# Kernel tuning notes

Measured on AMD Instinct MI355X. Metric: run time of the kernel, lower is better.

The kernel has to match this reference:

```python
import math
import jax, jax.numpy as jnp
import numpy as np

N, D, E, H = 4096, 512, 64, 8
LN_EPS = 1e-5


def setup_inputs() -> dict:
    key = jax.random.key(0)
    ks = jax.random.split(key, 6)
    return {
        "x": jax.random.normal(ks[0], (N, D), jnp.float32),
        "wq": jax.random.normal(ks[1], (H, D, E), jnp.float32) * 0.05,
        "wk": jax.random.normal(ks[2], (H, D, E), jnp.float32) * 0.05,
        "wv": jax.random.normal(ks[3], (H, D, E), jnp.float32) * 0.05,
        "w_mh": jax.random.normal(ks[4], (H * E, D), jnp.float32) * 0.05,
        "ln1_g": jnp.ones((D,), jnp.float32),
        "ln1_b": jnp.zeros((D,), jnp.float32),
        "ffn_w": jax.random.normal(ks[5], (D, D), jnp.float32) * 0.05,  # torch Linear weight [out,in]
        "ffn_b": jnp.zeros((D,), jnp.float32),
        "ln2_g": jnp.ones((D,), jnp.float32),
        "ln2_b": jnp.zeros((D,), jnp.float32),
    }


def _layernorm(y, g, b):
    m = y.mean(-1, keepdims=True)
    v = ((y - m) ** 2).mean(-1, keepdims=True)
    return (y - m) * jax.lax.rsqrt(v + LN_EPS) * g + b


def reference(x, wq, wk, wv, w_mh, ln1_g, ln1_b, ffn_w, ffn_b, ln2_g, ln2_b):
    dk = math.sqrt(wk.shape[-1])  # sqrt(embedding_size), as in the torch code
    q = jnp.einsum('nd,hde->hne', x, wq)  # [H,N,E]
    k = jnp.einsum('nd,hde->hne', x, wk)
    v = jnp.einsum('nd,hde->hne', x, wv)
    scores = jax.nn.softmax(jnp.einsum('hne,hme->hnm', q, k) / dk, axis=-1)  # [H,N,N]
    z = jnp.einsum('hnm,hme->hne', scores, v)  # [H,N,E]
    concat_z = jnp.transpose(z, (1, 0, 2)).reshape(x.shape[0], -1)  # [N, H*E]
    transformed_z = concat_z @ w_mh  # [N, D]
    normed_z = _layernorm(transformed_z + x, ln1_g, ln1_b)
    out = normed_z @ ffn_w.T + ffn_b  # nn.Linear
    return _layernorm(out + normed_z, ln2_g, ln2_b)
```

## Files before the change

### kernel.cpp

```cpp
#include <hip/hip_runtime.h>

#define NN 4096
#define DD 512
#define EE 64
#define HH 8

typedef _Float16 f16;
typedef f16 f16x4 __attribute__((ext_vector_type(4)));
typedef f16 f16x8 __attribute__((ext_vector_type(8)));
typedef float f32x4 __attribute__((ext_vector_type(4)));

__device__ __forceinline__ float hexp2(float x) { return __builtin_amdgcn_exp2f(x); }

__device__ void tile_transpose_cvt(const float* __restrict__ src, f16* __restrict__ dst,
                                   int R, int C, int bx, int by, int tid)
{
    __shared__ float t[32][33];
    const int tx = tid & 31, ty = tid >> 5;
    #pragma unroll
    for (int i = 0; i < 4; ++i) {
        int r = ty + i * 8;
        t[r][tx] = src[(size_t)(by + r) * C + bx + tx];
    }
    __syncthreads();
    #pragma unroll
    for (int i = 0; i < 4; ++i) {
        int c = ty + i * 8;
        dst[(size_t)(bx + c) * R + by + tx] = (f16)t[tx][c];
    }
}

__global__ __launch_bounds__(256) void prep_kernel(
    const float* __restrict__ x, const float* __restrict__ ffn_w,
    const float* __restrict__ wq, const float* __restrict__ wk, const float* __restrict__ wv,
    const float* __restrict__ w_mh,
    f16* __restrict__ xh, f16* __restrict__ ffnT, f16* __restrict__ wqkvT, f16* __restrict__ wmhT)
{
    const int job = blockIdx.y;
    const int tid = threadIdx.x;
    if (job == 0) {
        size_t i = ((size_t)blockIdx.x * 256 + tid) * 4;
        const size_t step = (size_t)256 * 256 * 4;
        for (; i < (size_t)NN * DD; i += step) {
            float4 t = *(const float4*)(x + i);
            f16x4 h = { (f16)t.x, (f16)t.y, (f16)t.z, (f16)t.w };
            *(f16x4*)(xh + i) = h;
        }
    } else if (job == 1) {
        size_t i = ((size_t)blockIdx.x * 256 + tid) * 4;
        float4 t = *(const float4*)(ffn_w + i);
        f16x4 h = { (f16)t.x, (f16)t.y, (f16)t.z, (f16)t.w };
        *(f16x4*)(ffnT + i) = h;
    } else if (job <= 4) {
        const float* src = (job == 2) ? wq : (job == 3) ? wk : wv;
        f16* dst = wqkvT + (size_t)(job - 2) * HH * EE * DD;
        const int z = blockIdx.x >> 5;
        const int tile = blockIdx.x & 31;
        tile_transpose_cvt(src + (size_t)z * DD * EE, dst + (size_t)z * DD * EE,
                           DD, EE, (tile & 1) * 32, (tile >> 1) * 32, tid);
    } else {
        const int tile = blockIdx.x;
        tile_transpose_cvt(w_mh, wmhT, DD, DD, (tile & 15) * 32, (tile >> 4) * 32, tid);
    }
}

__global__ __launch_bounds__(256) void qkv_mfma_kernel(
    const f16* __restrict__ A, const f16* __restrict__ BT,
    f16* __restrict__ qh, f16* __restrict__ kh, f16* __restrict__ vTh)
{
    __shared__ f16 As[64][72];
    __shared__ f16 Bs[64][72];
    const int tid = threadIdx.x;
    const int n0 = blockIdx.x * 64;
    const int cb = blockIdx.y;
    const int sel = cb >> 3, h = cb & 7;
    const f16* Arow = A + (size_t)n0 * DD;
    const f16* Brow = BT + (size_t)cb * 64 * DD;

    const int lane = tid & 63, wave = tid >> 6;
    const int l16 = lane & 15, quad = lane >> 4;
    const int m0 = wave * 16;

    f32x4 acc[4];
    #pragma unroll
    for (int t = 0; t < 4; ++t) acc[t] = (f32x4){0.f, 0.f, 0.f, 0.f};

    for (int kt = 0; kt < DD; kt += 64) {
        __syncthreads();
        #pragma unroll
        for (int i = 0; i < 2; ++i) {
            int idx = tid + i * 256;
            int r = idx >> 3, c8 = (idx & 7) * 8;
            *(f16x8*)(&As[r][c8]) = *(const f16x8*)(Arow + (size_t)r * DD + kt + c8);
            *(f16x8*)(&Bs[r][c8]) = *(const f16x8*)(Brow + (size_t)r * DD + kt + c8);
        }
        __syncthreads();
        #pragma unroll
        for (int kk = 0; kk < 64; kk += 32) {
            f16x8 a = *(const f16x8*)(&As[m0 + l16][kk + quad * 8]);
            #pragma unroll
            for (int t = 0; t < 4; ++t) {
                f16x8 b = *(const f16x8*)(&Bs[t * 16 + l16][kk + quad * 8]);
                acc[t] = __builtin_amdgcn_mfma_f32_16x16x32_f16(a, b, acc[t], 0, 0, 0);
            }
        }
    }

    if (sel == 2) {
        #pragma unroll
        for (int t = 0; t < 4; ++t) {
            int e = t * 16 + l16;
            #pragma unroll
            for (int r = 0; r < 4; ++r)
                vTh[((size_t)h * EE + e) * NN + n0 + m0 + quad * 4 + r] = (f16)acc[t][r];
        }
    } else {
        f16* o = (sel == 0) ? qh : kh;
        const float s = (sel == 0) ? 0.125f * 1.44269504088896f : 1.0f;
        #pragma unroll
        for (int r = 0; r < 4; ++r) {
            int row = n0 + m0 + quad * 4 + r;
            #pragma unroll
            for (int t = 0; t < 4; ++t)
                o[(size_t)h * NN * EE + (size_t)row * EE + t * 16 + l16] = (f16)(acc[t][r] * s);
        }
    }
}

#define BQ 128
#define BK 64
#define LK (BK + 12)

__global__ __launch_bounds__(256) void attn_mfma_kernel(
    const f16* __restrict__ q, const f16* __restrict__ k,
    const f16* __restrict__ vT, float* __restrict__ Opart, float* __restrict__ lpart)
{
    __shared__ f16 Ks[BK][LK];
    __shared__ f16 VsT[EE][LK];

    const int tid = threadIdx.x;
    const int h = blockIdx.y;
    const int n0 = blockIdx.x * BQ;
    const int sp = blockIdx.z;
    const int nsp = gridDim.z;
    const int wave = tid >> 6;
    const int lane = tid & 63;
    const int l16 = lane & 15;
    const int quad = lane >> 4;
    const int m0 = wave * 16;

    const f16* qh = q + (size_t)h * NN * EE;
    const f16* kh = k + (size_t)h * NN * EE;
    const f16* vh = vT + (size_t)h * NN * EE;

    f16x8 qf[2][2];
    #pragma unroll
    for (int s = 0; s < 2; ++s) {
        const f16* qb = qh + (size_t)(n0 + s * 64 + m0 + l16) * EE;
        qf[s][0] = *(const f16x8*)(qb + quad * 8);
        qf[s][1] = *(const f16x8*)(qb + 32 + quad * 8);
    }

    float lp[2] = {0.f, 0.f};
    f32x4 O[2][4];
    #pragma unroll
    for (int s = 0; s < 2; ++s)
        #pragma unroll
        for (int t = 0; t < 4; ++t) O[s][t] = (f32x4){0.f, 0.f, 0.f, 0.f};

    const int span = NN / nsp;
    const int k_begin = sp * span;
    const int k_end = k_begin + span;

    const int srow = tid >> 3, sc8 = (tid & 7) * 8;
    const int srow2 = (tid + 256) >> 3, sc82 = ((tid + 256) & 7) * 8;
    #define KPERM(kk_) (((kk_) & 0x23) | (((kk_) & 0x04) << 2) | (((kk_) & 0x18) >> 1))
    const int prow1 = KPERM(srow), prow2 = KPERM(srow2);

    f16x8 kr0 = *(const f16x8*)(kh + (size_t)(k_begin + srow) * EE + sc8);
    f16x8 kr1 = *(const f16x8*)(kh + (size_t)(k_begin + srow2) * EE + sc82);
    f16x8 vr0 = *(const f16x8*)(vh + (size_t)srow * NN + k_begin + sc8);
    f16x8 vr1 = *(const f16x8*)(vh + (size_t)srow2 * NN + k_begin + sc82);

    for (int kt = k_begin; kt < k_end; kt += BK) {
        __syncthreads();
        *(f16x8*)(&Ks[prow1][sc8]) = kr0;
        *(f16x8*)(&Ks[prow2][sc82]) = kr1;
        *(f16x8*)(&VsT[srow][sc8]) = vr0;
        *(f16x8*)(&VsT[srow2][sc82]) = vr1;
        __syncthreads();

        if (kt + BK < k_end) {
            kr0 = *(const f16x8*)(kh + (size_t)(kt + BK + srow) * EE + sc8);
            kr1 = *(const f16x8*)(kh + (size_t)(kt + BK + srow2) * EE + sc82);
            vr0 = *(const f16x8*)(vh + (size_t)srow * NN + kt + BK + sc8);
            vr1 = *(const f16x8*)(vh + (size_t)srow2 * NN + kt + BK + sc82);
        }

        f16x8 bf[2][2];
        #pragma unroll
        for (int t = 0; t < 4; ++t) {
            f16x8 a0 = *(const f16x8*)(&Ks[t * 16 + l16][quad * 8]);
            f16x8 a1 = *(const f16x8*)(&Ks[t * 16 + l16][32 + quad * 8]);
            #pragma unroll
            for (int s = 0; s < 2; ++s) {
                f32x4 st = {0.f, 0.f, 0.f, 0.f};
                st = __builtin_amdgcn_mfma_f32_16x16x32_f16(a0, qf[s][0], st, 0, 0, 0);
                st = __builtin_amdgcn_mfma_f32_16x16x32_f16(a1, qf[s][1], st, 0, 0, 0);
                float p0 = hexp2(st[0]);
                float p1 = hexp2(st[1]);
                float p2 = hexp2(st[2]);
                float p3 = hexp2(st[3]);
                lp[s] += (p0 + p1) + (p2 + p3);
                f16x8& b = bf[s][t >> 1];
                const int o = (t & 1) * 4;
                b[o + 0] = (f16)p0; b[o + 1] = (f16)p1;
                b[o + 2] = (f16)p2; b[o + 3] = (f16)p3;
            }
        }

        #pragma unroll
        for (int te = 0; te < 4; ++te) {
            f16x8 v0 = *(const f16x8*)(&VsT[te * 16 + l16][quad * 8]);
            f16x8 v1 = *(const f16x8*)(&VsT[te * 16 + l16][32 + quad * 8]);
            #pragma unroll
            for (int s = 0; s < 2; ++s) {
                O[s][te] = __builtin_amdgcn_mfma_f32_16x16x32_f16(v0, bf[s][0], O[s][te], 0, 0, 0);
                O[s][te] = __builtin_amdgcn_mfma_f32_16x16x32_f16(v1, bf[s][1], O[s][te], 0, 0, 0);
            }
        }
    }

    #pragma unroll
    for (int s = 0; s < 2; ++s) {
        float l = lp[s];
        l += __shfl_xor(l, 16);
        l += __shfl_xor(l, 32);
        const int row = n0 + s * 64 + m0 + l16;
        if (quad == 0)
            lpart[(size_t)sp * HH * NN + (size_t)h * NN + row] = l;
        float* obase = Opart + ((size_t)sp * NN + row) * DD + h * EE;
        #pragma unroll
        for (int te = 0; te < 4; ++te)
            *(f32x4*)(obase + te * 16 + quad * 4) = O[s][te];
    }
}

__global__ __launch_bounds__(256) void attn_combine_kernel(
    const float* __restrict__ Opart, const float* __restrict__ lpart, f16* __restrict__ zh, int nsp)
{
    const size_t idx = ((size_t)blockIdx.x * 256 + threadIdx.x) * 8;
    const int n = (int)(idx >> 9);
    const int h = (int)((idx & 511) >> 6);
    float l = 0.f;
    for (int s = 0; s < nsp; ++s) l += lpart[(size_t)s * HH * NN + (size_t)h * NN + n];
    const float inv = 1.f / l;
    f32x4 a0 = {0.f,0.f,0.f,0.f}, a1 = {0.f,0.f,0.f,0.f};
    for (int s = 0; s < nsp; ++s) {
        a0 += *(const f32x4*)(Opart + (size_t)s * NN * DD + idx);
        a1 += *(const f32x4*)(Opart + (size_t)s * NN * DD + idx + 4);
    }
    f16x8 o;
    #pragma unroll
    for (int i = 0; i < 4; ++i) {
        o[i]     = (f16)(a0[i] * inv);
        o[i + 4] = (f16)(a1[i] * inv);
    }
    *(f16x8*)(zh + idx) = o;
}

__global__ __launch_bounds__(256) void gemm_mfma_kernel(
    const f16* __restrict__ A, const f16* __restrict__ BT,
    const float* __restrict__ bias, const float* __restrict__ resid32,
    const f16* __restrict__ resid16, float* __restrict__ out)
{
    __shared__ f16 As[64][72];
    __shared__ f16 Bs[64][72];
    const int tid = threadIdx.x;
    const int n0 = blockIdx.x * 64;
    const int j0 = blockIdx.y * 64;
    const f16* Arow = A + (size_t)n0 * DD;
    const f16* Brow = BT + (size_t)j0 * DD;

    const int lane = tid & 63, wave = tid >> 6;
    const int l16 = lane & 15, quad = lane >> 4;
    const int m0 = wave * 16;

    f32x4 acc[4];
    #pragma unroll
    for (int t = 0; t < 4; ++t) acc[t] = (f32x4){0.f, 0.f, 0.f, 0.f};

    for (int kt = 0; kt < DD; kt += 64) {
        __syncthreads();
        #pragma unroll
        for (int i = 0; i < 2; ++i) {
            int idx = tid + i * 256;
            int r = idx >> 3, c8 = (idx & 7) * 8;
            *(f16x8*)(&As[r][c8]) = *(const f16x8*)(Arow + (size_t)r * DD + kt + c8);
            *(f16x8*)(&Bs[r][c8]) = *(const f16x8*)(Brow + (size_t)r * DD + kt + c8);
        }
        __syncthreads();
        #pragma unroll
        for (int kk = 0; kk < 64; kk += 32) {
            f16x8 a = *(const f16x8*)(&As[m0 + l16][kk + quad * 8]);
            #pragma unroll
            for (int t = 0; t < 4; ++t) {
                f16x8 b = *(const f16x8*)(&Bs[t * 16 + l16][kk + quad * 8]);
                acc[t] = __builtin_amdgcn_mfma_f32_16x16x32_f16(a, b, acc[t], 0, 0, 0);
            }
        }
    }

    #pragma unroll
    for (int r = 0; r < 4; ++r) {
        int row = n0 + m0 + quad * 4 + r;
        #pragma unroll
        for (int t = 0; t < 4; ++t) {
            int col = j0 + t * 16 + l16;
            float v = acc[t][r];
            if (bias)    v += bias[col];
            if (resid32) v += resid32[(size_t)row * DD + col];
            if (resid16) v += (float)resid16[(size_t)row * DD + col];
            out[(size_t)row * DD + col] = v;
        }
    }
}

__global__ __launch_bounds__(256) void ln_kernel(
    const float* __restrict__ y, const float* __restrict__ g, const float* __restrict__ b,
    f16* __restrict__ oh, float* __restrict__ of)
{
    const int lane = threadIdx.x & 63, wave = threadIdx.x >> 6;
    const int row = blockIdx.x * 4 + wave;
    const float* yr = y + (size_t)row * DD;
    f32x4 v0 = *(const f32x4*)(yr + lane * 4);
    f32x4 v1 = *(const f32x4*)(yr + 256 + lane * 4);
    float s = (v0[0] + v0[1]) + (v0[2] + v0[3]) + (v1[0] + v1[1]) + (v1[2] + v1[3]);
    float q = (v0[0]*v0[0] + v0[1]*v0[1]) + (v0[2]*v0[2] + v0[3]*v0[3])
            + (v1[0]*v1[0] + v1[1]*v1[1]) + (v1[2]*v1[2] + v1[3]*v1[3]);
    #pragma unroll
    for (int o = 1; o < 64; o <<= 1) { s += __shfl_xor(s, o); q += __shfl_xor(q, o); }
    float mean = s * (1.f / DD);
    float var = q * (1.f / DD) - mean * mean;
    float inv = rsqrtf(var + 1e-5f);

    f32x4 g0 = *(const f32x4*)(g + lane * 4);
    f32x4 g1 = *(const f32x4*)(g + 256 + lane * 4);
    f32x4 b0 = *(const f32x4*)(b + lane * 4);
    f32x4 b1 = *(const f32x4*)(b + 256 + lane * 4);
    f32x4 o0, o1;
    #pragma unroll
    for (int i = 0; i < 4; ++i) {
        o0[i] = (v0[i] - mean) * inv * g0[i] + b0[i];
        o1[i] = (v1[i] - mean) * inv * g1[i] + b1[i];
    }
    if (oh) {
        f16x4 h0 = { (f16)o0[0], (f16)o0[1], (f16)o0[2], (f16)o0[3] };
        f16x4 h1 = { (f16)o1[0], (f16)o1[1], (f16)o1[2], (f16)o1[3] };
        *(f16x4*)(oh + (size_t)row * DD + lane * 4) = h0;
        *(f16x4*)(oh + (size_t)row * DD + 256 + lane * 4) = h1;
    }
    if (of) {
        *(f32x4*)(of + (size_t)row * DD + lane * 4) = o0;
        *(f32x4*)(of + (size_t)row * DD + 256 + lane * 4) = o1;
    }
}

extern "C" void kernel_launch(void* const* d_in, const int* in_sizes, int n_in,
                              void* d_out, int out_size, void* d_ws, size_t ws_size,
                              hipStream_t stream) {
    const float* x     = (const float*)d_in[0];
    const float* wq    = (const float*)d_in[1];
    const float* wk    = (const float*)d_in[2];
    const float* wv    = (const float*)d_in[3];
    const float* w_mh  = (const float*)d_in[4];
    const float* ln1_g = (const float*)d_in[5];
    const float* ln1_b = (const float*)d_in[6];
    const float* ffn_w = (const float*)d_in[7];
    const float* ffn_b = (const float*)d_in[8];
    const float* ln2_g = (const float*)d_in[9];
    const float* ln2_b = (const float*)d_in[10];
    float* out = (float*)d_out;

    const size_t poolHalfs = (size_t)3 * HH * EE * DD + 2 * (size_t)DD * DD
                           + 3 * (size_t)HH * NN * EE + 2 * (size_t)NN * DD;
    int SP = 2;
    {
        size_t need4 = ((size_t)4 * NN * DD + 4 * HH * NN) * 4 + poolHalfs * 2 + 1024;
        size_t need3 = ((size_t)3 * NN * DD + 3 * HH * NN) * 4 + poolHalfs * 2 + 1024;
        if (ws_size >= need4) SP = 4; else if (ws_size >= need3) SP = 3;
    }

    char* base = (char*)d_ws;
    float* Opart = (float*)base;
    float* lpart = Opart + (size_t)SP * NN * DD;
    f16* xh   = (f16*)base;
    float* y  = (float*)base;
    size_t regionA = ((size_t)SP * NN * DD + (size_t)SP * HH * NN) * sizeof(float);
    regionA = (regionA + 255) & ~(size_t)255;
    f16* p = (f16*)(base + regionA);
    f16* wqkvT  = p; p += (size_t)3 * HH * EE * DD;
    f16* wmhT   = p; p += (size_t)DD * DD;
    f16* ffnT   = p; p += (size_t)DD * DD;
    f16* qh     = p; p += (size_t)HH * NN * EE;
    f16* kh     = p; p += (size_t)HH * NN * EE;
    f16* vTh    = p; p += (size_t)HH * NN * EE;
    f16* zh     = p; p += (size_t)NN * DD;
    f16* nzh    = p; p += (size_t)NN * DD;

    prep_kernel<<<dim3(256, 6), 256, 0, stream>>>(x, ffn_w, wq, wk, wv, w_mh,
                                                  xh, ffnT, wqkvT, wmhT);

    qkv_mfma_kernel<<<dim3(NN / 64, 24), 256, 0, stream>>>(xh, wqkvT, qh, kh, vTh);
    attn_mfma_kernel<<<dim3(NN / BQ, HH, SP), 256, 0, stream>>>(qh, kh, vTh, Opart, lpart);
    attn_combine_kernel<<<dim3(NN * DD / 2048), 256, 0, stream>>>(Opart, lpart, zh, SP);
    gemm_mfma_kernel<<<dim3(NN / 64, DD / 64), 256, 0, stream>>>(zh, wmhT, nullptr, x, nullptr, y);
    ln_kernel<<<dim3(NN / 4), 256, 0, stream>>>(y, ln1_g, ln1_b, nzh, nullptr);
    gemm_mfma_kernel<<<dim3(NN / 64, DD / 64), 256, 0, stream>>>(nzh, ffnT, ffn_b, nullptr, nzh, y);
    ln_kernel<<<dim3(NN / 4), 256, 0, stream>>>(y, ln2_g, ln2_b, nullptr, out);
}
```

Baseline: 186.5 us.

## Store normalized fp16 attention partials, raise split count, prefetch GEMM tiles

Attention partial outputs are now normalized by their local row sum and stored as fp16 instead of fp32. The combine kernel re-weights each split by its share of the total sum, which halves partial-output traffic and lets the split count rise to 8 when workspace allows. The QKV and output GEMMs now prefetch the next K tile into registers while the current one is computed, and the V-transpose store is vectorized. Storing partials in fp16 adds some rounding error, and more splits add combine work.

Result: no change. 188.7 us (+1.2%).

```diff
diff --git a/kernel.cpp b/kernel.cpp
--- a/kernel.cpp
+++ b/kernel.cpp
@@ -81,20 +81,31 @@
     const int l16 = lane & 15, quad = lane >> 4;
     const int m0 = wave * 16;
 
+    const int r1 = tid >> 3, c1 = (tid & 7) * 8;
+    const int r2 = (tid + 256) >> 3, c2 = ((tid + 256) & 7) * 8;
+
     f32x4 acc[4];
     #pragma unroll
     for (int t = 0; t < 4; ++t) acc[t] = (f32x4){0.f, 0.f, 0.f, 0.f};
 
+    f16x8 a1 = *(const f16x8*)(Arow + (size_t)r1 * DD + c1);
+    f16x8 a2 = *(const f16x8*)(Arow + (size_t)r2 * DD + c2);
+    f16x8 b1 = *(const f16x8*)(Brow + (size_t)r1 * DD + c1);
+    f16x8 b2 = *(const f16x8*)(Brow + (size_t)r2 * DD + c2);
+
     for (int kt = 0; kt < DD; kt += 64) {
         __syncthreads();
-        #pragma unroll
-        for (int i = 0; i < 2; ++i) {
-            int idx = tid + i * 256;
-            int r = idx >> 3, c8 = (idx & 7) * 8;
-            *(f16x8*)(&As[r][c8]) = *(const f16x8*)(Arow + (size_t)r * DD + kt + c8);
-            *(f16x8*)(&Bs[r][c8]) = *(const f16x8*)(Brow + (size_t)r * DD + kt + c8);
-        }
-        __syncthreads();
+        *(f16x8*)(&As[r1][c1]) = a1;
+        *(f16x8*)(&As[r2][c2]) = a2;
+        *(f16x8*)(&Bs[r1][c1]) = b1;
+        *(f16x8*)(&Bs[r2][c2]) = b2;
+        __syncthreads();
+        if (kt + 64 < DD) {
+            a1 = *(const f16x8*)(Arow + (size_t)r1 * DD + kt + 64 + c1);
+            a2 = *(const f16x8*)(Arow + (size_t)r2 * DD + kt + 64 + c2);
+            b1 = *(const f16x8*)(Brow + (size_t)r1 * DD + kt + 64 + c1);
+            b2 = *(const f16x8*)(Brow + (size_t)r2 * DD + kt + 64 + c2);
+        }
         #pragma unroll
         for (int kk = 0; kk < 64; kk += 32) {
             f16x8 a = *(const f16x8*)(&As[m0 + l16][kk + quad * 8]);
@@ -110,9 +121,8 @@
         #pragma unroll
         for (int t = 0; t < 4; ++t) {
             int e = t * 16 + l16;
-            #pragma unroll
-            for (int r = 0; r < 4; ++r)
-                vTh[((size_t)h * EE + e) * NN + n0 + m0 + quad * 4 + r] = (f16)acc[t][r];
+            f16x4 v = { (f16)acc[t][0], (f16)acc[t][1], (f16)acc[t][2], (f16)acc[t][3] };
+            *(f16x4*)(vTh + ((size_t)h * EE + e) * NN + n0 + m0 + quad * 4) = v;
         }
     } else {
         f16* o = (sel == 0) ? qh : kh;
@@ -133,7 +143,7 @@
 
 __global__ __launch_bounds__(256) void attn_mfma_kernel(
     const f16* __restrict__ q, const f16* __restrict__ k,
-    const f16* __restrict__ vT, float* __restrict__ Opart, float* __restrict__ lpart)
+    const f16* __restrict__ vT, f16* __restrict__ Opart, float* __restrict__ lpart)
 {
     __shared__ f16 Ks[BK][LK];
     __shared__ f16 VsT[EE][LK];
@@ -239,34 +249,43 @@
         const int row = n0 + s * 64 + m0 + l16;
         if (quad == 0)
             lpart[(size_t)sp * HH * NN + (size_t)h * NN + row] = l;
-        float* obase = Opart + ((size_t)sp * NN + row) * DD + h * EE;
-        #pragma unroll
-        for (int te = 0; te < 4; ++te)
-            *(f32x4*)(obase + te * 16 + quad * 4) = O[s][te];
+        const float inv = 1.f / l;
+        f16* obase = Opart + ((size_t)sp * NN + row) * DD + h * EE;
+        #pragma unroll
+        for (int te = 0; te < 4; ++te) {
+            f16x4 v = { (f16)(O[s][te][0] * inv), (f16)(O[s][te][1] * inv),
+                        (f16)(O[s][te][2] * inv), (f16)(O[s][te][3] * inv) };
+            *(f16x4*)(obase + te * 16 + quad * 4) = v;
+        }
     }
 }
 
 __global__ __launch_bounds__(256) void attn_combine_kernel(
-    const float* __restrict__ Opart, const float* __restrict__ lpart, f16* __restrict__ zh, int nsp)
+    const f16* __restrict__ Opart, const float* __restrict__ lpart, f16* __restrict__ zh, int nsp)
 {
     const size_t idx = ((size_t)blockIdx.x * 256 + threadIdx.x) * 8;
     const int n = (int)(idx >> 9);
     const int h = (int)((idx & 511) >> 6);
-    float l = 0.f;
-    for (int s = 0; s < nsp; ++s) l += lpart[(size_t)s * HH * NN + (size_t)h * NN + n];
-    const float inv = 1.f / l;
-    f32x4 a0 = {0.f,0.f,0.f,0.f}, a1 = {0.f,0.f,0.f,0.f};
+    float lw[8];
+    float lsum = 0.f;
     for (int s = 0; s < nsp; ++s) {
-        a0 += *(const f32x4*)(Opart + (size_t)s * NN * DD + idx);
-        a1 += *(const f32x4*)(Opart + (size_t)s * NN * DD + idx + 4);
-    }
-    f16x8 o;
-    #pragma unroll
-    for (int i = 0; i < 4; ++i) {
-        o[i]     = (f16)(a0[i] * inv);
-        o[i + 4] = (f16)(a1[i] * inv);
-    }
-    *(f16x8*)(zh + idx) = o;
+        lw[s] = lpart[(size_t)s * HH * NN + (size_t)h * NN + n];
+        lsum += lw[s];
+    }
+    const float inv = 1.f / lsum;
+    float acc[8];
+    #pragma unroll
+    for (int i = 0; i < 8; ++i) acc[i] = 0.f;
+    for (int s = 0; s < nsp; ++s) {
+        f16x8 o = *(const f16x8*)(Opart + (size_t)s * NN * DD + idx);
+        const float w = lw[s] * inv;
+        #pragma unroll
+        for (int i = 0; i < 8; ++i) acc[i] += w * (float)o[i];
+    }
+    f16x8 z;
+    #pragma unroll
+    for (int i = 0; i < 8; ++i) z[i] = (f16)acc[i];
+    *(f16x8*)(zh + idx) = z;
 }
 
 __global__ __launch_bounds__(256) void gemm_mfma_kernel(
@@ -286,20 +305,31 @@
     const int l16 = lane & 15, quad = lane >> 4;
     const int m0 = wave * 16;
 
+    const int r1 = tid >> 3, c1 = (tid & 7) * 8;
+    const int r2 = (tid + 256) >> 3, c2 = ((tid + 256) & 7) * 8;
+
     f32x4 acc[4];
     #pragma unroll
     for (int t = 0; t < 4; ++t) acc[t] = (f32x4){0.f, 0.f, 0.f, 0.f};
 
+    f16x8 a1 = *(const f16x8*)(Arow + (size_t)r1 * DD + c1);
+    f16x8 a2 = *(const f16x8*)(Arow + (size_t)r2 * DD + c2);
+    f16x8 b1 = *(const f16x8*)(Brow + (size_t)r1 * DD + c1);
+    f16x8 b2 = *(const f16x8*)(Brow + (size_t)r2 * DD + c2);
+
     for (int kt = 0; kt < DD; kt += 64) {
         __syncthreads();
-        #pragma unroll
-        for (int i = 0; i < 2; ++i) {
-            int idx = tid + i * 256;
-            int r = idx >> 3, c8 = (idx & 7) * 8;
-            *(f16x8*)(&As[r][c8]) = *(const f16x8*)(Arow + (size_t)r * DD + kt + c8);
-            *(f16x8*)(&Bs[r][c8]) = *(const f16x8*)(Brow + (size_t)r * DD + kt + c8);
-        }
-        __syncthreads();
+        *(f16x8*)(&As[r1][c1]) = a1;
+        *(f16x8*)(&As[r2][c2]) = a2;
+        *(f16x8*)(&Bs[r1][c1]) = b1;
+        *(f16x8*)(&Bs[r2][c2]) = b2;
+        __syncthreads();
+        if (kt + 64 < DD) {
+            a1 = *(const f16x8*)(Arow + (size_t)r1 * DD + kt + 64 + c1);
+            a2 = *(const f16x8*)(Arow + (size_t)r2 * DD + kt + 64 + c2);
+            b1 = *(const f16x8*)(Brow + (size_t)r1 * DD + kt + 64 + c1);
+            b2 = *(const f16x8*)(Brow + (size_t)r2 * DD + kt + 64 + c2);
+        }
         #pragma unroll
         for (int kk = 0; kk < 64; kk += 32) {
             f16x8 a = *(const f16x8*)(&As[m0 + l16][kk + quad * 8]);
@@ -382,21 +412,21 @@
     const float* ln2_b = (const float*)d_in[10];
     float* out = (float*)d_out;
 
-    const size_t poolHalfs = (size_t)3 * HH * EE * DD + 2 * (size_t)DD * DD
-                           + 3 * (size_t)HH * NN * EE + 2 * (size_t)NN * DD;
+    const size_t poolBytes = ((size_t)3 * HH * EE * DD + 2 * (size_t)DD * DD
+                            + 3 * (size_t)HH * NN * EE + 2 * (size_t)NN * DD) * 2;
     int SP = 2;
     {
-        size_t need4 = ((size_t)4 * NN * DD + 4 * HH * NN) * 4 + poolHalfs * 2 + 1024;
-        size_t need3 = ((size_t)3 * NN * DD + 3 * HH * NN) * 4 + poolHalfs * 2 + 1024;
-        if (ws_size >= need4) SP = 4; else if (ws_size >= need3) SP = 3;
+        size_t need8 = (size_t)8 * NN * DD * 2 + (size_t)8 * HH * NN * 4 + poolBytes + 4096;
+        size_t need4 = (size_t)4 * NN * DD * 2 + (size_t)4 * HH * NN * 4 + poolBytes + 4096;
+        if (ws_size >= need8) SP = 8; else if (ws_size >= need4) SP = 4;
     }
 
     char* base = (char*)d_ws;
-    float* Opart = (float*)base;
-    float* lpart = Opart + (size_t)SP * NN * DD;
+    f16* Opart = (f16*)base;
+    float* lpart = (float*)(base + (size_t)SP * NN * DD * 2);
     f16* xh   = (f16*)base;
     float* y  = (float*)base;
-    size_t regionA = ((size_t)SP * NN * DD + (size_t)SP * HH * NN) * sizeof(float);
+    size_t regionA = (size_t)SP * NN * DD * 2 + (size_t)SP * HH * NN * 4;
     regionA = (regionA + 255) & ~(size_t)255;
     f16* p = (f16*)(base + regionA);
     f16* wqkvT  = p; p += (size_t)3 * HH * EE * DD;
```
